# Optimization experiments

Measured on AMD Instinct MI355X. Metric: run time of the kernel, lower is better.

## Reference

```python
import jax, jax.numpy as jnp
import numpy as np

B, T, D_MODEL, D_HIDDEN, MAX_SEQLEN = 4, 2048, 1024, 1024, 2048


def setup_inputs() -> dict:
    key = jax.random.key(0)
    ks = jax.random.split(key, 8)
    scale = 0.02  # keep exp() and linear outputs in a sane range
    return {
        "q": jax.random.normal(ks[0], (B, T, D_MODEL), dtype=jnp.float32),
        "k": jax.random.normal(ks[1], (B, T, D_MODEL), dtype=jnp.float32),
        "v": jax.random.normal(ks[2], (B, T, D_MODEL), dtype=jnp.float32),
        "Wq": jax.random.normal(ks[3], (D_HIDDEN, D_MODEL), dtype=jnp.float32) * scale,
        "Wk": jax.random.normal(ks[4], (D_HIDDEN, D_MODEL), dtype=jnp.float32) * scale,
        "Wv": jax.random.normal(ks[5], (D_HIDDEN, D_MODEL), dtype=jnp.float32) * scale,
        "Wo": jax.random.normal(ks[6], (D_MODEL, D_HIDDEN), dtype=jnp.float32) * scale,
        "W_bias": jax.random.normal(ks[7], (MAX_SEQLEN, MAX_SEQLEN), dtype=jnp.float32) * scale,
    }


def reference(q, k, v, Wq, Wk, Wv, Wo, W_bias):
    Ti = q.shape[1]
    Tj = k.shape[1]
    # Linear projections (torch Linear: x @ W.T), bias=False
    Q = jnp.einsum('btm,hm->bth', q, Wq)
    K = jnp.einsum('btm,hm->bth', k, Wk)
    V = jnp.einsum('btm,hm->bth', v, Wv)
    pos_bias = W_bias[:Ti, :Tj][None]              # (1, Ti, Tj)
    # Faithful to original: max over dim 0 (batch dim for K, singleton dim for pos_bias)
    max_key = jnp.max(K, axis=0, keepdims=True)    # (1, Tj, Dh)
    max_pos_bias = jnp.max(pos_bias, axis=0, keepdims=True)  # == pos_bias (dim 0 is size 1)
    exp_key = jnp.exp(K - max_key)                 # (B, Tj, Dh)
    exp_pos_bias = jnp.exp(pos_bias - max_pos_bias)  # all-ones, kept for faithfulness
    num = jnp.einsum('bij,bjd->bid', exp_pos_bias, exp_key * V)
    den = jnp.einsum('bij,bjd->bid', exp_pos_bias, exp_key)
    Yt = jax.nn.sigmoid(Q) * num / den             # (B, Ti, Dh)
    return jnp.einsum('bth,mh->btm', Yt, Wo)
```

## Files before the change

### kernel.cpp

```cpp
#include <hip/hip_runtime.h>
#include <hip/hip_bf16.h>

typedef __bf16 bf16;
typedef __bf16 bf16x8 __attribute__((ext_vector_type(8)));
typedef __bf16 bf16x4 __attribute__((ext_vector_type(4)));
typedef __bf16 bf16x2 __attribute__((ext_vector_type(2)));
typedef float f32x4 __attribute__((ext_vector_type(4)));

#define B_   4
#define T_   2048
#define DM_  1024
#define DH_  1024
#define MROWS (B_ * T_)

struct CvtJob { const float* src; bf16* dst; int nf4; };
struct CvtArgs { CvtJob job[3]; };

__global__ __launch_bounds__(256) void cvt_kernel(CvtArgs args) {
  CvtJob jb = args.job[blockIdx.y];
  int f4 = blockIdx.x * 1024 + threadIdx.x * 2;
  if (f4 >= jb.nf4) return;
  const float4* s = (const float4*)jb.src;
  float4 a0 = s[f4];
  float4 a1 = s[f4 + 1];
  float4 b0 = s[f4 + 512];
  float4 b1 = s[f4 + 513];
  bf16x8 oa, ob;
  oa[0] = (bf16)a0.x; oa[1] = (bf16)a0.y; oa[2] = (bf16)a0.z; oa[3] = (bf16)a0.w;
  oa[4] = (bf16)a1.x; oa[5] = (bf16)a1.y; oa[6] = (bf16)a1.z; oa[7] = (bf16)a1.w;
  ob[0] = (bf16)b0.x; ob[1] = (bf16)b0.y; ob[2] = (bf16)b0.z; ob[3] = (bf16)b0.w;
  ob[4] = (bf16)b1.x; ob[5] = (bf16)b1.y; ob[6] = (bf16)b1.z; ob[7] = (bf16)b1.w;
  *(bf16x8*)(jb.dst + (size_t)f4 * 4) = oa;
  *(bf16x8*)(jb.dst + (size_t)(f4 + 512) * 4) = ob;
}

struct GemmJob { const void* A; const bf16* Bw; float* Cf; bf16* Cb; int mode; };
struct GemmArgs { GemmJob job[4]; int N; int K; };

template <bool AF32>
__global__ __launch_bounds__(256) void gemm_bt(GemmArgs ga) {
  const GemmJob jb = ga.job[blockIdx.z];
  const int N = ga.N, K = ga.K;
  __shared__ bf16 As[128 * 64];
  __shared__ bf16 Bs[128 * 64];

  const int tid  = threadIdx.x;
  const int lane = tid & 63;
  const int wave = tid >> 6;
  const int wm   = (wave >> 1) * 64;
  const int wn   = (wave & 1) * 64;

  const int f   = blockIdx.y * 8 + blockIdx.x;
  const int xcd = f & 7;
  const int j   = f >> 3;
  const int bn  = j & 7;
  const int bm  = (j >> 3) * 8 + xcd;
  const int tileM = bm * 128;
  const int tileN = bn * 128;

  f32x4 acc[4][4] = {};

  const int sr = lane >> 3;
  const int sc = (lane & 7) ^ sr;

  for (int k0 = 0; k0 < K; k0 += 64) {
    if (AF32) {
      const float* Af = (const float*)jb.A;
      float4 av[4][2];
#pragma unroll
      for (int l = 0; l < 4; ++l) {
        int grp = wave * 4 + l;
        int row = grp * 8 + sr;
        const float4* ga4 = (const float4*)(Af + (size_t)(tileM + row) * K + k0 + sc * 8);
        av[l][0] = ga4[0];
        av[l][1] = ga4[1];
      }
#pragma unroll
      for (int l = 0; l < 4; ++l) {
        int grp = wave * 4 + l;
        bf16x8 w;
        w[0] = (bf16)av[l][0].x; w[1] = (bf16)av[l][0].y;
        w[2] = (bf16)av[l][0].z; w[3] = (bf16)av[l][0].w;
        w[4] = (bf16)av[l][1].x; w[5] = (bf16)av[l][1].y;
        w[6] = (bf16)av[l][1].z; w[7] = (bf16)av[l][1].w;
        *(bf16x8*)&As[grp * 512 + lane * 8] = w;
      }
    } else {
      const bf16* Ab = (const bf16*)jb.A;
#pragma unroll
      for (int l = 0; l < 4; ++l) {
        int grp = wave * 4 + l;
        int row = grp * 8 + sr;
        const bf16* gaadr = Ab + (size_t)(tileM + row) * K + k0 + sc * 8;
        __builtin_amdgcn_global_load_lds(
            (const __attribute__((address_space(1))) void*)gaadr,
            (__attribute__((address_space(3))) void*)&As[grp * 512], 16, 0, 0);
      }
    }
#pragma unroll
    for (int l = 0; l < 4; ++l) {
      int grp = wave * 4 + l;
      int row = grp * 8 + sr;
      const bf16* gbadr = jb.Bw + (size_t)(tileN + row) * K + k0 + sc * 8;
      __builtin_amdgcn_global_load_lds(
          (const __attribute__((address_space(1))) void*)gbadr,
          (__attribute__((address_space(3))) void*)&Bs[grp * 512], 16, 0, 0);
    }
    __syncthreads();

    const int quad = lane >> 4;
#pragma unroll
    for (int s = 0; s < 2; ++s) {
      bf16x8 af[4], bfr[4];
#pragma unroll
      for (int mt = 0; mt < 4; ++mt) {
        int row = wm + mt * 16 + (lane & 15);
        int chunk = (s * 4 + quad) ^ (row & 7);
        af[mt] = *(const bf16x8*)&As[row * 64 + chunk * 8];
      }
#pragma unroll
      for (int nt = 0; nt < 4; ++nt) {
        int row = wn + nt * 16 + (lane & 15);
        int chunk = (s * 4 + quad) ^ (row & 7);
        bfr[nt] = *(const bf16x8*)&Bs[row * 64 + chunk * 8];
      }
#pragma unroll
      for (int mt = 0; mt < 4; ++mt)
#pragma unroll
        for (int nt = 0; nt < 4; ++nt)
          acc[mt][nt] = __builtin_amdgcn_mfma_f32_16x16x32_bf16(
              af[mt], bfr[nt], acc[mt][nt], 0, 0, 0);
    }
    __syncthreads();
  }

  const int cn = lane & 15;
  const int cr = (lane >> 4) * 4;
  if (jb.mode == 0) {
#pragma unroll
    for (int mt = 0; mt < 4; ++mt)
#pragma unroll
      for (int nt = 0; nt < 4; ++nt)
#pragma unroll
        for (int r = 0; r < 4; ++r) {
          int row = tileM + wm + mt * 16 + cr + r;
          int col = tileN + wn + nt * 16 + cn;
          jb.Cf[(size_t)row * N + col] = acc[mt][nt][r];
        }
  } else if (jb.mode == 1) {
#pragma unroll
    for (int mt = 0; mt < 4; ++mt)
#pragma unroll
      for (int nt = 0; nt < 4; ++nt)
#pragma unroll
        for (int r = 0; r < 4; ++r) {
          int row = tileM + wm + mt * 16 + cr + r;
          int col = tileN + wn + nt * 16 + cn;
          jb.Cb[(size_t)row * N + col] =
              (bf16)(1.f / (1.f + __expf(-acc[mt][nt][r])));
        }
  } else {
#pragma unroll
    for (int mt = 0; mt < 4; ++mt)
#pragma unroll
      for (int nt = 0; nt < 4; ++nt)
#pragma unroll
        for (int r = 0; r < 4; ++r) {
          int row = tileM + wm + mt * 16 + cr + r;
          int col = tileN + wn + nt * 16 + cn;
          jb.Cb[(size_t)row * N + col] = (bf16)acc[mt][nt][r];
        }
  }
}

__global__ __launch_bounds__(256) void reduce_kv(
    const bf16* __restrict__ Kb, const bf16* __restrict__ Vb,
    float* __restrict__ num, float* __restrict__ den) {
  const int d  = (blockIdx.x * 256 + threadIdx.x) * 2;
  const int j0 = blockIdx.y * 16;
  const size_t bs = (size_t)T_ * DH_;
  float n[4][2] = {}, e[4][2] = {};
  for (int jj = j0; jj < j0 + 16; ++jj) {
    size_t off = (size_t)jj * DH_ + d;
    float kf[4][2], vf[4][2];
#pragma unroll
    for (int b = 0; b < 4; ++b) {
      bf16x2 kk = *(const bf16x2*)(Kb + off + b * bs);
      bf16x2 vv = *(const bf16x2*)(Vb + off + b * bs);
      kf[b][0] = (float)kk[0]; kf[b][1] = (float)kk[1];
      vf[b][0] = (float)vv[0]; vf[b][1] = (float)vv[1];
    }
#pragma unroll
    for (int c = 0; c < 2; ++c) {
      float m = fmaxf(fmaxf(kf[0][c], kf[1][c]), fmaxf(kf[2][c], kf[3][c]));
#pragma unroll
      for (int b = 0; b < 4; ++b) {
        float w = __expf(kf[b][c] - m);
        e[b][c] += w;
        n[b][c] += w * vf[b][c];
      }
    }
  }
#pragma unroll
  for (int b = 0; b < 4; ++b)
#pragma unroll
    for (int c = 0; c < 2; ++c) {
      atomicAdd(&num[b * DH_ + d + c], n[b][c]);
      atomicAdd(&den[b * DH_ + d + c], e[b][c]);
    }
}

__global__ __launch_bounds__(256) void scale_wo(
    const float* __restrict__ Wo, const float* __restrict__ num,
    const float* __restrict__ den, bf16* __restrict__ Wos) {
  int i = (blockIdx.x * 256 + threadIdx.x) * 4;
  int h = i & (DH_ - 1);
  float4 w = *(const float4*)(Wo + i);
#pragma unroll
  for (int b = 0; b < 4; ++b) {
    float4 nu = *(const float4*)(num + b * DH_ + h);
    float4 de = *(const float4*)(den + b * DH_ + h);
    bf16x4 o;
    o[0] = (bf16)(w.x * nu.x / de.x);
    o[1] = (bf16)(w.y * nu.y / de.y);
    o[2] = (bf16)(w.z * nu.z / de.z);
    o[3] = (bf16)(w.w * nu.w / de.w);
    *(bf16x4*)(Wos + (size_t)b * DH_ * DM_ + i) = o;
  }
}

extern "C" void kernel_launch(void* const* d_in, const int* in_sizes, int n_in,
                              void* d_out, int out_size, void* d_ws, size_t ws_size,
                              hipStream_t stream) {
  const float* q  = (const float*)d_in[0];
  const float* k  = (const float*)d_in[1];
  const float* v  = (const float*)d_in[2];
  const float* Wq = (const float*)d_in[3];
  const float* Wk = (const float*)d_in[4];
  const float* Wv = (const float*)d_in[5];
  const float* Wo = (const float*)d_in[6];
  float* out = (float*)d_out;

  char* ws = (char*)d_ws;
  size_t off = 0;
  auto alloc = [&](size_t bytes) {
    char* p = ws + off;
    off += (bytes + 255) & ~(size_t)255;
    return p;
  };
  const size_t actN = (size_t)MROWS * DM_;
  const size_t wN   = (size_t)DH_ * DM_;

  bf16* Wqb = (bf16*)alloc(wN * 2);
  bf16* Wkb = (bf16*)alloc(wN * 2);
  bf16* Wvb = (bf16*)alloc(wN * 2);
  bf16* Kb  = (bf16*)alloc(actN * 2);
  bf16* Vb  = (bf16*)alloc(actN * 2);
  bf16* Yb  = (bf16*)alloc(actN * 2);
  bf16* Wos = (bf16*)alloc(4 * wN * 2);
  float* num = (float*)alloc(B_ * DH_ * 4);
  float* den = (float*)alloc(B_ * DH_ * 4);

  CvtArgs ca;
  ca.job[0] = {Wq, Wqb, (int)(wN / 4)};
  ca.job[1] = {Wk, Wkb, (int)(wN / 4)};
  ca.job[2] = {Wv, Wvb, (int)(wN / 4)};
  cvt_kernel<<<dim3(wN / 4 / 1024, 3), 256, 0, stream>>>(ca);

  hipMemsetAsync(num, 0, 2 * B_ * DH_ * sizeof(float), stream);

  GemmArgs g1;
  g1.N = DH_; g1.K = DM_;
  g1.job[0] = {k, Wkb, nullptr, Kb, 2};
  g1.job[1] = {v, Wvb, nullptr, Vb, 2};
  g1.job[2] = {q, Wqb, nullptr, Yb, 1};
  g1.job[3] = {nullptr, nullptr, nullptr, nullptr, 0};
  gemm_bt<true><<<dim3(8, MROWS / 128, 3), 256, 0, stream>>>(g1);

  reduce_kv<<<dim3(2, 128), 256, 0, stream>>>(Kb, Vb, num, den);

  scale_wo<<<dim3(wN / 4 / 256), 256, 0, stream>>>(Wo, num, den, Wos);

  GemmArgs g2;
  g2.N = DM_; g2.K = DH_;
  for (int b = 0; b < 4; ++b)
    g2.job[b] = {Yb + (size_t)b * T_ * DH_, Wos + (size_t)b * wN,
                 out + (size_t)b * T_ * DM_, nullptr, 0};
  gemm_bt<false><<<dim3(8, T_ / 128, 4), 256, 0, stream>>>(g2);
}
```

Baseline: 295.3 us.

## Pre-convert activations to bf16 and apply num/den ratio to Y instead of Wo

Activations q, k and v are now converted to bf16 up front in one batched convert kernel, so the projection GEMM uses only the async global-to-LDS load path and no longer converts in registers. The per-batch scaling of Wo is replaced by an elementwise kernel that multiplies Y by num/den, which lets the output GEMM share a single bf16 Wo. The reduction kernel is widened to 8-element vector loads with fewer blocks. The trade is an extra full read and write of the activations in bf16 plus an extra pass over Y, in exchange for simpler GEMM loads.

```diff
diff --git a/kernel.cpp b/kernel.cpp
--- a/kernel.cpp
+++ b/kernel.cpp
@@ -4,40 +4,43 @@
 typedef __bf16 bf16;
 typedef __bf16 bf16x8 __attribute__((ext_vector_type(8)));
 typedef __bf16 bf16x4 __attribute__((ext_vector_type(4)));
-typedef __bf16 bf16x2 __attribute__((ext_vector_type(2)));
 typedef float f32x4 __attribute__((ext_vector_type(4)));
 
 #define B_   4
 #define T_   2048
 #define DM_  1024
 #define DH_  1024
-#define MROWS (B_ * T_)
+#define MROWS 8192
 
 struct CvtJob { const float* src; bf16* dst; int nf4; };
-struct CvtArgs { CvtJob job[3]; };
+struct CvtArgs { CvtJob job[7]; };
 
 __global__ __launch_bounds__(256) void cvt_kernel(CvtArgs args) {
   CvtJob jb = args.job[blockIdx.y];
-  int f4 = blockIdx.x * 1024 + threadIdx.x * 2;
-  if (f4 >= jb.nf4) return;
+  int base = blockIdx.x * 2048;
+  if (base >= jb.nf4) return;
+  int t2 = threadIdx.x * 2;
   const float4* s = (const float4*)jb.src;
-  float4 a0 = s[f4];
-  float4 a1 = s[f4 + 1];
-  float4 b0 = s[f4 + 512];
-  float4 b1 = s[f4 + 513];
-  bf16x8 oa, ob;
-  oa[0] = (bf16)a0.x; oa[1] = (bf16)a0.y; oa[2] = (bf16)a0.z; oa[3] = (bf16)a0.w;
-  oa[4] = (bf16)a1.x; oa[5] = (bf16)a1.y; oa[6] = (bf16)a1.z; oa[7] = (bf16)a1.w;
-  ob[0] = (bf16)b0.x; ob[1] = (bf16)b0.y; ob[2] = (bf16)b0.z; ob[3] = (bf16)b0.w;
-  ob[4] = (bf16)b1.x; ob[5] = (bf16)b1.y; ob[6] = (bf16)b1.z; ob[7] = (bf16)b1.w;
-  *(bf16x8*)(jb.dst + (size_t)f4 * 4) = oa;
-  *(bf16x8*)(jb.dst + (size_t)(f4 + 512) * 4) = ob;
-}
-
-struct GemmJob { const void* A; const bf16* Bw; float* Cf; bf16* Cb; int mode; };
+  float4 a[4][2];
+#pragma unroll
+  for (int u = 0; u < 4; ++u) {
+    a[u][0] = s[base + u * 512 + t2];
+    a[u][1] = s[base + u * 512 + t2 + 1];
+  }
+#pragma unroll
+  for (int u = 0; u < 4; ++u) {
+    bf16x8 o;
+    o[0] = (bf16)a[u][0].x; o[1] = (bf16)a[u][0].y;
+    o[2] = (bf16)a[u][0].z; o[3] = (bf16)a[u][0].w;
+    o[4] = (bf16)a[u][1].x; o[5] = (bf16)a[u][1].y;
+    o[6] = (bf16)a[u][1].z; o[7] = (bf16)a[u][1].w;
+    *(bf16x8*)(jb.dst + ((size_t)base + u * 512 + t2) * 4) = o;
+  }
+}
+
+struct GemmJob { const bf16* A; const bf16* Bw; float* Cf; bf16* Cb; int mode; };
 struct GemmArgs { GemmJob job[4]; int N; int K; };
 
-template <bool AF32>
 __global__ __launch_bounds__(256) void gemm_bt(GemmArgs ga) {
   const GemmJob jb = ga.job[blockIdx.z];
   const int N = ga.N, K = ga.K;
@@ -64,43 +67,14 @@
   const int sc = (lane & 7) ^ sr;
 
   for (int k0 = 0; k0 < K; k0 += 64) {
-    if (AF32) {
-      const float* Af = (const float*)jb.A;
-      float4 av[4][2];
-#pragma unroll
-      for (int l = 0; l < 4; ++l) {
-        int grp = wave * 4 + l;
-        int row = grp * 8 + sr;
-        const float4* ga4 = (const float4*)(Af + (size_t)(tileM + row) * K + k0 + sc * 8);
-        av[l][0] = ga4[0];
-        av[l][1] = ga4[1];
-      }
-#pragma unroll
-      for (int l = 0; l < 4; ++l) {
-        int grp = wave * 4 + l;
-        bf16x8 w;
-        w[0] = (bf16)av[l][0].x; w[1] = (bf16)av[l][0].y;
-        w[2] = (bf16)av[l][0].z; w[3] = (bf16)av[l][0].w;
-        w[4] = (bf16)av[l][1].x; w[5] = (bf16)av[l][1].y;
-        w[6] = (bf16)av[l][1].z; w[7] = (bf16)av[l][1].w;
-        *(bf16x8*)&As[grp * 512 + lane * 8] = w;
-      }
-    } else {
-      const bf16* Ab = (const bf16*)jb.A;
-#pragma unroll
-      for (int l = 0; l < 4; ++l) {
-        int grp = wave * 4 + l;
-        int row = grp * 8 + sr;
-        const bf16* gaadr = Ab + (size_t)(tileM + row) * K + k0 + sc * 8;
-        __builtin_amdgcn_global_load_lds(
-            (const __attribute__((address_space(1))) void*)gaadr,
-            (__attribute__((address_space(3))) void*)&As[grp * 512], 16, 0, 0);
-      }
-    }
 #pragma unroll
     for (int l = 0; l < 4; ++l) {
       int grp = wave * 4 + l;
       int row = grp * 8 + sr;
+      const bf16* gaadr = jb.A + (size_t)(tileM + row) * K + k0 + sc * 8;
+      __builtin_amdgcn_global_load_lds(
+          (const __attribute__((address_space(1))) void*)gaadr,
+          (__attribute__((address_space(3))) void*)&As[grp * 512], 16, 0, 0);
       const bf16* gbadr = jb.Bw + (size_t)(tileN + row) * K + k0 + sc * 8;
       __builtin_amdgcn_global_load_lds(
           (const __attribute__((address_space(1))) void*)gbadr,
@@ -176,22 +150,22 @@
 __global__ __launch_bounds__(256) void reduce_kv(
     const bf16* __restrict__ Kb, const bf16* __restrict__ Vb,
     float* __restrict__ num, float* __restrict__ den) {
-  const int d  = (blockIdx.x * 256 + threadIdx.x) * 2;
-  const int j0 = blockIdx.y * 16;
+  const int d  = (threadIdx.x & 127) * 8;
+  const int j0 = blockIdx.x * 32 + (threadIdx.x >> 7) * 16;
   const size_t bs = (size_t)T_ * DH_;
-  float n[4][2] = {}, e[4][2] = {};
+  float n[4][8] = {}, e[4][8] = {};
   for (int jj = j0; jj < j0 + 16; ++jj) {
     size_t off = (size_t)jj * DH_ + d;
-    float kf[4][2], vf[4][2];
+    float kf[4][8], vf[4][8];
 #pragma unroll
     for (int b = 0; b < 4; ++b) {
-      bf16x2 kk = *(const bf16x2*)(Kb + off + b * bs);
-      bf16x2 vv = *(const bf16x2*)(Vb + off + b * bs);
-      kf[b][0] = (float)kk[0]; kf[b][1] = (float)kk[1];
-      vf[b][0] = (float)vv[0]; vf[b][1] = (float)vv[1];
-    }
-#pragma unroll
-    for (int c = 0; c < 2; ++c) {
+      bf16x8 kk = *(const bf16x8*)(Kb + off + b * bs);
+      bf16x8 vv = *(const bf16x8*)(Vb + off + b * bs);
+#pragma unroll
+      for (int c = 0; c < 8; ++c) { kf[b][c] = (float)kk[c]; vf[b][c] = (float)vv[c]; }
+    }
+#pragma unroll
+    for (int c = 0; c < 8; ++c) {
       float m = fmaxf(fmaxf(kf[0][c], kf[1][c]), fmaxf(kf[2][c], kf[3][c]));
 #pragma unroll
       for (int b = 0; b < 4; ++b) {
@@ -204,29 +178,35 @@
 #pragma unroll
   for (int b = 0; b < 4; ++b)
 #pragma unroll
-    for (int c = 0; c < 2; ++c) {
+    for (int c = 0; c < 8; ++c) {
       atomicAdd(&num[b * DH_ + d + c], n[b][c]);
       atomicAdd(&den[b * DH_ + d + c], e[b][c]);
     }
 }
 
-__global__ __launch_bounds__(256) void scale_wo(
-    const float* __restrict__ Wo, const float* __restrict__ num,
-    const float* __restrict__ den, bf16* __restrict__ Wos) {
-  int i = (blockIdx.x * 256 + threadIdx.x) * 4;
-  int h = i & (DH_ - 1);
-  float4 w = *(const float4*)(Wo + i);
-#pragma unroll
-  for (int b = 0; b < 4; ++b) {
-    float4 nu = *(const float4*)(num + b * DH_ + h);
-    float4 de = *(const float4*)(den + b * DH_ + h);
-    bf16x4 o;
-    o[0] = (bf16)(w.x * nu.x / de.x);
-    o[1] = (bf16)(w.y * nu.y / de.y);
-    o[2] = (bf16)(w.z * nu.z / de.z);
-    o[3] = (bf16)(w.w * nu.w / de.w);
-    *(bf16x4*)(Wos + (size_t)b * DH_ * DM_ + i) = o;
-  }
+__global__ __launch_bounds__(256) void mul_ratio(
+    bf16* __restrict__ Yb, const float* __restrict__ num,
+    const float* __restrict__ den) {
+  size_t i = ((size_t)blockIdx.x * 256 + threadIdx.x) * 8;
+  int h = (int)(i & (DH_ - 1));
+  int b = (int)(i >> 21);
+  bf16x8 y = *(bf16x8*)(Yb + i);
+  const float* nu = num + b * DH_ + h;
+  const float* de = den + b * DH_ + h;
+  float4 n0 = *(const float4*)nu;
+  float4 n1 = *(const float4*)(nu + 4);
+  float4 d0 = *(const float4*)de;
+  float4 d1 = *(const float4*)(de + 4);
+  bf16x8 o;
+  o[0] = (bf16)((float)y[0] * n0.x / d0.x);
+  o[1] = (bf16)((float)y[1] * n0.y / d0.y);
+  o[2] = (bf16)((float)y[2] * n0.z / d0.z);
+  o[3] = (bf16)((float)y[3] * n0.w / d0.w);
+  o[4] = (bf16)((float)y[4] * n1.x / d1.x);
+  o[5] = (bf16)((float)y[5] * n1.y / d1.y);
+  o[6] = (bf16)((float)y[6] * n1.z / d1.z);
+  o[7] = (bf16)((float)y[7] * n1.w / d1.w);
+  *(bf16x8*)(Yb + i) = o;
 }
 
 extern "C" void kernel_launch(void* const* d_in, const int* in_sizes, int n_in,
@@ -251,40 +231,46 @@
   const size_t actN = (size_t)MROWS * DM_;
   const size_t wN   = (size_t)DH_ * DM_;
 
+  bf16* qb  = (bf16*)alloc(actN * 2);
+  bf16* kb  = (bf16*)alloc(actN * 2);
+  bf16* vb  = (bf16*)alloc(actN * 2);
   bf16* Wqb = (bf16*)alloc(wN * 2);
   bf16* Wkb = (bf16*)alloc(wN * 2);
   bf16* Wvb = (bf16*)alloc(wN * 2);
+  bf16* Wob = (bf16*)alloc(wN * 2);
   bf16* Kb  = (bf16*)alloc(actN * 2);
   bf16* Vb  = (bf16*)alloc(actN * 2);
   bf16* Yb  = (bf16*)alloc(actN * 2);
-  bf16* Wos = (bf16*)alloc(4 * wN * 2);
   float* num = (float*)alloc(B_ * DH_ * 4);
   float* den = (float*)alloc(B_ * DH_ * 4);
 
   CvtArgs ca;
-  ca.job[0] = {Wq, Wqb, (int)(wN / 4)};
-  ca.job[1] = {Wk, Wkb, (int)(wN / 4)};
-  ca.job[2] = {Wv, Wvb, (int)(wN / 4)};
-  cvt_kernel<<<dim3(wN / 4 / 1024, 3), 256, 0, stream>>>(ca);
+  ca.job[0] = {q,  qb,  (int)(actN / 4)};
+  ca.job[1] = {k,  kb,  (int)(actN / 4)};
+  ca.job[2] = {v,  vb,  (int)(actN / 4)};
+  ca.job[3] = {Wq, Wqb, (int)(wN / 4)};
+  ca.job[4] = {Wk, Wkb, (int)(wN / 4)};
+  ca.job[5] = {Wv, Wvb, (int)(wN / 4)};
+  ca.job[6] = {Wo, Wob, (int)(wN / 4)};
+  cvt_kernel<<<dim3(actN / 4 / 2048, 7), 256, 0, stream>>>(ca);
 
   hipMemsetAsync(num, 0, 2 * B_ * DH_ * sizeof(float), stream);
 
   GemmArgs g1;
   g1.N = DH_; g1.K = DM_;
-  g1.job[0] = {k, Wkb, nullptr, Kb, 2};
-  g1.job[1] = {v, Wvb, nullptr, Vb, 2};
-  g1.job[2] = {q, Wqb, nullptr, Yb, 1};
+  g1.job[0] = {kb, Wkb, nullptr, Kb, 2};
+  g1.job[1] = {vb, Wvb, nullptr, Vb, 2};
+  g1.job[2] = {qb, Wqb, nullptr, Yb, 1};
   g1.job[3] = {nullptr, nullptr, nullptr, nullptr, 0};
-  gemm_bt<true><<<dim3(8, MROWS / 128, 3), 256, 0, stream>>>(g1);
-
-  reduce_kv<<<dim3(2, 128), 256, 0, stream>>>(Kb, Vb, num, den);
-
-  scale_wo<<<dim3(wN / 4 / 256), 256, 0, stream>>>(Wo, num, den, Wos);
+  gemm_bt<<<dim3(8, MROWS / 128, 3), 256, 0, stream>>>(g1);
+
+  reduce_kv<<<dim3(64), 256, 0, stream>>>(Kb, Vb, num, den);
+
+  mul_ratio<<<dim3(actN / 8 / 256), 256, 0, stream>>>(Yb, num, den);
 
   GemmArgs g2;
   g2.N = DM_; g2.K = DH_;
-  for (int b = 0; b < 4; ++b)
-    g2.job[b] = {Yb + (size_t)b * T_ * DH_, Wos + (size_t)b * wN,
-                 out + (size_t)b * T_ * DM_, nullptr, 0};
-  gemm_bt<false><<<dim3(8, T_ / 128, 4), 256, 0, stream>>>(g2);
-}
+  g2.job[0] = {Yb, Wob, out, nullptr, 0};
+  g2.job[1] = g2.job[2] = g2.job[3] = {nullptr, nullptr, nullptr, nullptr, 0};
+  gemm_bt<<<dim3(8, MROWS / 128, 1), 256, 0, stream>>>(g2);
+}
```

New measurement: 347.8 us. 1.18x slower.
